# Kernel optimization log

Hardware: AMD Instinct MI355X
Metric: run time of the kernel (lower is better)

The kernel has to match this reference:

```python
import jax, jax.numpy as jnp
import numpy as np

B, S, T, H, E = 256, 512, 16, 1024, 512  # batch, src_len, trg_steps, hidden, emb_dim


def setup_inputs() -> dict:
    key = jax.random.key(0)
    ks = jax.random.split(key, 10)
    rn = lambda k, sh: jax.random.normal(k, sh, dtype=jnp.float32) * 0.05
    return {
        "trg_emb": rn(ks[0], (B, T, E)),
        "h0": rn(ks[1], (B, H)),
        "c0": rn(ks[2], (B, H)),
        "ctx": rn(ks[3], (B, S, H)),
        "src_len": jax.random.randint(ks[4], (B,), 1, S + 1, dtype=jnp.int32),
        "W_ih": rn(ks[5], (4 * H, E + H)),  # input-feeding: lstm in = emb + hidden
        "W_hh": rn(ks[6], (4 * H, H)),
        "b_ih": jnp.zeros((4 * H,), jnp.float32),
        "b_hh": jnp.zeros((4 * H,), jnp.float32),
        "W_in": rn(ks[7], (H, H)),    # attention linear_in (no bias)
        "W_out": rn(ks[8], (H, 2 * H)),  # attention linear_out (no bias)
    }


def reference(trg_emb, h0, c0, ctx, src_len, W_ih, W_hh, b_ih, b_hh, W_in, W_out):
    # mask[b, s] = s < src_len[b]
    mask = jnp.arange(S)[None, :] < src_len[:, None]  # (B, S)
    neg = jnp.float32(-1e9)

    def step(carry, emb_t):
        h, c, h_tilde = carry  # each (B, H); emb_t (B, E)
        # input feeding: concat target embedding with previous attentional vector
        x = jnp.concatenate([emb_t, h_tilde], axis=1)  # (B, E+H)
        gates = x @ W_ih.T + b_ih + h @ W_hh.T + b_hh  # (B, 4H), pytorch gate order i,f,g,o
        i, f, g, o = jnp.split(gates, 4, axis=1)
        i = jax.nn.sigmoid(i); f = jax.nn.sigmoid(f)
        g = jnp.tanh(g);       o = jax.nn.sigmoid(o)
        c = f * c + i * g
        h = o * jnp.tanh(c)
        # Luong soft-dot attention with src_len masking
        target = h @ W_in.T                                # (B, H)
        scores = jnp.einsum('bsh,bh->bs', ctx, target)     # (B, S)
        scores = jnp.where(mask, scores, neg)
        attn = jax.nn.softmax(scores, axis=-1)
        weighted = jnp.einsum('bs,bsh->bh', attn, ctx)     # (B, H)
        h_tilde = jnp.tanh(jnp.concatenate([weighted, h], axis=1) @ W_out.T)
        return (h, c, h_tilde), h_tilde

    # initial h_tilde = init_hidden[0] (per the original code)
    (h_f, c_f, _), hs = jax.lax.scan(step, (h0, c0, h0), jnp.swapaxes(trg_emb, 0, 1))
    output = jnp.swapaxes(hs, 0, 1)  # (B, T, H)
    return output, h_f, c_f
```

## Files before the change

### kernel.cpp

```cpp
#include <hip/hip_runtime.h>
#include <cstdint>
#include <cstddef>


#define B_ 256
#define S_ 512
#define T_ 16
#define H_ 1024
#define E_ 512
#define NBUF 4

typedef unsigned short u16;
using short8 = __attribute__((ext_vector_type(8))) short;
using f32x4  = __attribute__((ext_vector_type(4))) float;

__device__ __forceinline__ float bf2f(u16 u) {
  union { uint32_t i; float f; } v; v.i = ((uint32_t)u) << 16; return v.f;
}
__device__ __forceinline__ u16 f2bf(float f) {
  union { uint32_t i; float f; } v; v.f = f;
  uint32_t r = v.i + 0x7fffu + ((v.i >> 16) & 1u);
  return (u16)(r >> 16);
}
__device__ __forceinline__ float sigmoidf_(float x) { return 1.f / (1.f + __expf(-x)); }

__device__ __forceinline__ void gload_lds16(const void* g, void* l) {
  __builtin_amdgcn_global_load_lds(
      (const __attribute__((address_space(1))) void*)g,
      (__attribute__((address_space(3))) void*)l, 16, 0, 0);
}

struct Reg3 { const u16* A; int lda; const u16* B; int ldb; int kt; };

template <int EPI>
__global__ __launch_bounds__(128) void gemm_k(Reg3 r0, Reg3 r1, Reg3 r2,
                                              int nmb,
                                              float* __restrict__ Cf,
                                              u16* __restrict__ Cb,
                                              const float* __restrict__ bsum,
                                              float* __restrict__ cst,
                                              float* __restrict__ h32o,
                                              u16* __restrict__ hbfo,
                                              const int tstep) {
  __shared__ u16 smA[NBUF][64 * 64];
  __shared__ u16 smB[NBUF][64 * 64];
  const int tid = threadIdx.x;
  const int lane = tid & 63;
  const int wave = tid >> 6;
  const int m0 = (blockIdx.x % nmb) * 64;
  const int n0 = (blockIdx.x / nmb) * 64;
  const int row16 = lane & 15;
  const int kg = lane >> 4;
  const int nt = r0.kt + r1.kt + r2.kt;

  auto stage = [&](int ti, int buf) {
    const int k01 = r0.kt + r1.kt;
    const u16* Ap = (ti < r0.kt) ? r0.A : (ti < k01) ? r1.A : r2.A;
    const u16* Bp = (ti < r0.kt) ? r0.B : (ti < k01) ? r1.B : r2.B;
    const int lda = (ti < r0.kt) ? r0.lda : (ti < k01) ? r1.lda : r2.lda;
    const int ldb = (ti < r0.kt) ? r0.ldb : (ti < k01) ? r1.ldb : r2.ldb;
    const int base = (ti < r0.kt) ? 0 : (ti < k01) ? r0.kt : k01;
    const int kr = (ti - base) << 6;
#pragma unroll
    for (int j = 0; j < 4; ++j) {
      const int c = j * 128 + tid;
      const int row = c >> 3, q = c & 7;
      gload_lds16(Ap + (size_t)(m0 + row) * lda + kr + ((q ^ (row & 7)) << 3),
                  (char*)&smA[buf][0] + (size_t)(j * 128 + wave * 64) * 16);
    }
#pragma unroll
    for (int j = 0; j < 4; ++j) {
      const int c = j * 128 + tid;
      const int row = c >> 3, q = c & 7;
      gload_lds16(Bp + (size_t)(n0 + row) * ldb + kr + ((q ^ (row & 7)) << 3),
                  (char*)&smB[buf][0] + (size_t)(j * 128 + wave * 64) * 16);
    }
  };

  f32x4 acc[4][2] = {};
  stage(0, 0);
  if (nt > 1) stage(1, 1);
  for (int ti = 0; ti < nt; ++ti) {
    const int buf = ti & 3;
    if (ti + 2 < nt) {
      stage(ti + 2, (ti + 2) & 3);
      asm volatile("s_waitcnt vmcnt(16)" ::: "memory");
    } else if (ti + 1 < nt) {
      asm volatile("s_waitcnt vmcnt(8)" ::: "memory");
    } else {
      asm volatile("s_waitcnt vmcnt(0)" ::: "memory");
    }
    __builtin_amdgcn_s_barrier();
    __builtin_amdgcn_sched_barrier(0);
#pragma unroll
    for (int ks = 0; ks < 2; ++ks) {
      short8 af[4], bfr[2];
#pragma unroll
      for (int mi = 0; mi < 4; ++mi) {
        const int R = mi * 16 + row16;
        af[mi] = *(const short8*)((const char*)&smA[buf][0] +
                                  (size_t)(((R << 3) | ((ks * 4 + kg) ^ (R & 7))) << 4));
      }
#pragma unroll
      for (int ni = 0; ni < 2; ++ni) {
        const int R = wave * 32 + ni * 16 + row16;
        bfr[ni] = *(const short8*)((const char*)&smB[buf][0] +
                                   (size_t)(((R << 3) | ((ks * 4 + kg) ^ (R & 7))) << 4));
      }
      asm volatile("s_waitcnt lgkmcnt(0)" ::: "memory");
      __builtin_amdgcn_sched_barrier(0);
#pragma unroll
      for (int mi = 0; mi < 4; ++mi)
#pragma unroll
        for (int ni = 0; ni < 2; ++ni)
          acc[mi][ni] = __builtin_amdgcn_mfma_f32_16x16x32_bf16(af[mi], bfr[ni], acc[mi][ni], 0, 0, 0);
      __builtin_amdgcn_sched_barrier(0);
    }
  }
#pragma unroll
  for (int mi = 0; mi < 4; ++mi) {
#pragma unroll
    for (int ni = 0; ni < 2; ++ni) {
#pragma unroll
      for (int r = 0; r < 4; ++r) {
        const int row = m0 + mi * 16 + (kg << 2) + r;
        const int col = n0 + wave * 32 + ni * 16 + row16;
        float v = acc[mi][ni][r];
        if (EPI == 2) {
          float tv = tanhf(v);
          Cf[(size_t)row * (T_ * H_) + (size_t)tstep * H_ + col] = tv;
          Cb[row * H_ + col] = f2bf(tv);
        } else {
          v += bsum[col];
          float v1 = __shfl_xor(v, 1);
          float v2 = __shfl_xor(v, 2);
          float v3 = __shfl_xor(v, 3);
          if ((lane & 3) == 0) {
            const int u = col >> 2;
            float iv = sigmoidf_(v);
            float fv = sigmoidf_(v1);
            float gv = tanhf(v2);
            float ov = sigmoidf_(v3);
            float cn = fv * cst[row * H_ + u] + iv * gv;
            float hn = ov * tanhf(cn);
            cst[row * H_ + u] = cn;
            h32o[row * H_ + u] = hn;
            hbfo[row * H_ + u] = f2bf(hn);
          }
        }
      }
    }
  }
}

__device__ __forceinline__ int fidx(int lane, int j) {
  return (j << 6) + ((lane + (j << 2)) & 63);
}

__global__ __launch_bounds__(1024) void attn_k(const u16* __restrict__ hbf,
                                               const u16* __restrict__ WinT,
                                               const u16* __restrict__ ctxb,
                                               const int* __restrict__ src_len,
                                               u16* __restrict__ wwbf) {
  __shared__ float hsm[1024];
  __shared__ float tgtp[1024 + 64];
  __shared__ float facc[8][1024];
  __shared__ float fm[16], fl[16];
  const int b = blockIdx.x;
  const int tid = threadIdx.x;
  const int lane = tid & 63;
  const int wave = tid >> 6;
  const int len = src_len[b];

  hsm[tid] = bf2f(hbf[b * H_ + tid]);
  __syncthreads();

  {
    float a = 0.f;
    const u16* wp = WinT + tid * 8;
    for (int k8 = 0; k8 < 128; ++k8) {
      short8 wv = *(const short8*)(wp + (size_t)k8 * 8192);
      float4 h0v = *(const float4*)&hsm[k8 * 8];
      float4 h1v = *(const float4*)&hsm[k8 * 8 + 4];
      a += bf2f((u16)wv[0]) * h0v.x + bf2f((u16)wv[1]) * h0v.y
         + bf2f((u16)wv[2]) * h0v.z + bf2f((u16)wv[3]) * h0v.w
         + bf2f((u16)wv[4]) * h1v.x + bf2f((u16)wv[5]) * h1v.y
         + bf2f((u16)wv[6]) * h1v.z + bf2f((u16)wv[7]) * h1v.w;
    }
    tgtp[tid + (tid >> 4)] = a;
  }
  __syncthreads();

  float tg[16];
#pragma unroll
  for (int j = 0; j < 16; ++j) tg[j] = tgtp[lane * 17 + j];

  float m = -1e30f, l = 0.f;
  float acc[16];
#pragma unroll
  for (int j = 0; j < 16; ++j) acc[j] = 0.f;

  for (int s = wave; s < len; s += 16) {
    const u16* cr = ctxb + (((size_t)b * S_ + s) << 10) + (lane << 4);
    short8 v1 = *(const short8*)cr;
    short8 v2 = *(const short8*)(cr + 8);
    float cf[16];
#pragma unroll
    for (int j = 0; j < 8; ++j) { cf[j] = bf2f((u16)v1[j]); cf[8 + j] = bf2f((u16)v2[j]); }
    float x = 0.f;
#pragma unroll
    for (int j = 0; j < 16; ++j) x += cf[j] * tg[j];
#pragma unroll
    for (int off = 1; off < 64; off <<= 1) x += __shfl_xor(x, off);
    if (x > m) {
      float sc_ = __expf(m - x);
      l *= sc_;
#pragma unroll
      for (int j = 0; j < 16; ++j) acc[j] *= sc_;
      m = x;
    }
    float p = __expf(x - m);
    l += p;
#pragma unroll
    for (int j = 0; j < 16; ++j) acc[j] += p * cf[j];
  }

  if (wave >= 8) {
#pragma unroll
    for (int j = 0; j < 16; ++j) facc[wave - 8][fidx(lane, j)] = acc[j];
    if (lane == 0) { fm[wave] = m; fl[wave] = l; }
  }
  __syncthreads();
  if (wave < 8) {
    float pm = fm[8 + wave];
    float pl = fl[8 + wave];
    float M = fmaxf(m, pm);
    float e1 = __expf(m - M);
    float e2 = __expf(pm - M);
#pragma unroll
    for (int j = 0; j < 16; ++j) {
      float pv = facc[wave][fidx(lane, j)];
      facc[wave][fidx(lane, j)] = acc[j] * e1 + pv * e2;
    }
    if (lane == 0) { fm[wave] = M; fl[wave] = l * e1 + pl * e2; }
  }
  __syncthreads();
  float mstar = -1e30f;
#pragma unroll
  for (int w = 0; w < 8; ++w) mstar = fmaxf(mstar, fm[w]);
  float lsum = 0.f, asum = 0.f;
  const int ri = fidx(tid >> 4, tid & 15);
#pragma unroll
  for (int w = 0; w < 8; ++w) {
    float e = __expf(fm[w] - mstar);
    lsum += fl[w] * e;
    asum += facc[w][ri] * e;
  }
  wwbf[b * H_ + tid] = f2bf(asum / lsum);
}

__global__ __launch_bounds__(256) void convert_all(
    const float* __restrict__ W_ih, const float* __restrict__ W_hh,
    const float* __restrict__ W_in, const float* __restrict__ W_out,
    const float* __restrict__ trg_emb, const float* __restrict__ ctx,
    const float* __restrict__ b_ih, const float* __restrict__ b_hh,
    const float* __restrict__ h0, const float* __restrict__ c0,
    u16* __restrict__ wWih, u16* __restrict__ wWhh, u16* __restrict__ wWinT,
    u16* __restrict__ wWout, u16* __restrict__ wemb, u16* __restrict__ wctx,
    float* __restrict__ wbsum, u16* __restrict__ wh0, u16* __restrict__ whtbf,
    float* __restrict__ wc) {
  const int gtid = blockIdx.x * 256 + threadIdx.x;
  const int GSZ = 2048 * 256;
  auto cvt4 = [](float4 v) {
    ushort4 o; o.x = f2bf(v.x); o.y = f2bf(v.y); o.z = f2bf(v.z); o.w = f2bf(v.w);
    return o;
  };
  for (int i = gtid; i < 1572864; i += GSZ) {
    const int r = i / 384, c4 = i - r * 384;
    const int rp = ((r & 1023) << 2) + (r >> 10);
    ((ushort4*)wWih)[(size_t)rp * 384 + c4] = cvt4(((const float4*)W_ih)[i]);
  }
  for (int i = gtid; i < 1048576; i += GSZ) {
    const int r = i >> 8, c4 = i & 255;
    const int rp = ((r & 1023) << 2) + (r >> 10);
    ((ushort4*)wWhh)[(size_t)rp * 256 + c4] = cvt4(((const float4*)W_hh)[i]);
  }
  for (int i = gtid; i < 524288; i += GSZ)
    ((ushort4*)wWout)[i] = cvt4(((const float4*)W_out)[i]);
  for (int i = gtid; i < 524288; i += GSZ)
    ((ushort4*)wemb)[i] = cvt4(((const float4*)trg_emb)[i]);
  for (int i = gtid; i < 131072; i += GSZ) {
    const int n = i >> 7, k8 = i & 127;
    const float* s = W_in + (size_t)n * 1024 + k8 * 8;
    ushort4* d = (ushort4*)(wWinT + (size_t)k8 * 8192 + n * 8);
    d[0] = cvt4(*(const float4*)s);
    d[1] = cvt4(*(const float4*)(s + 4));
  }
  for (int i = gtid; i < 33554432; i += GSZ)
    ((ushort4*)wctx)[i] = cvt4(((const float4*)ctx)[i]);
  if (gtid < 4096) {
    const int cp = ((gtid & 1023) << 2) + (gtid >> 10);
    wbsum[cp] = b_ih[gtid] + b_hh[gtid];
  }
  for (int i = gtid; i < 262144; i += GSZ) {
    u16 hb = f2bf(h0[i]);
    wh0[i] = hb;
    whtbf[i] = hb;
    wc[i] = c0[i];
  }
}

extern "C" void kernel_launch(void* const* d_in, const int* in_sizes, int n_in,
                              void* d_out, int out_size, void* d_ws, size_t ws_size,
                              hipStream_t stream) {
  const float* trg_emb = (const float*)d_in[0];
  const float* h0      = (const float*)d_in[1];
  const float* c0      = (const float*)d_in[2];
  const float* ctx     = (const float*)d_in[3];
  const int*   src_len = (const int*)d_in[4];
  const float* W_ih    = (const float*)d_in[5];
  const float* W_hh    = (const float*)d_in[6];
  const float* b_ih    = (const float*)d_in[7];
  const float* b_hh    = (const float*)d_in[8];
  const float* W_in    = (const float*)d_in[9];
  const float* W_out   = (const float*)d_in[10];
  float* out = (float*)d_out;

  char* w = (char*)d_ws;
  size_t off = 0;
  auto alloc = [&](size_t bytes) { char* p = w + off; off += bytes; return p; };
  u16*   wWih  = (u16*)  alloc(12582912);
  u16*   wWhh  = (u16*)  alloc(8388608);
  u16*   wWinT = (u16*)  alloc(2097152);
  u16*   wWout = (u16*)  alloc(4194304);
  u16*   wemb  = (u16*)  alloc(4194304);
  float* wbsum = (float*)alloc(16384);
  float* wh32  = (float*)alloc(1048576);
  float* wc    = (float*)alloc(1048576);
  u16*   wh0   = (u16*)  alloc(524288);
  u16*   wh1   = (u16*)  alloc(524288);
  u16*   whtbf = (u16*)  alloc(524288);
  u16*   wwbf  = (u16*)  alloc(524288);
  u16*   wctx  = (u16*)  alloc(268435456);
  (void)ws_size;

  convert_all<<<dim3(2048), dim3(256), 0, stream>>>(
      W_ih, W_hh, W_in, W_out, trg_emb, ctx, b_ih, b_hh, h0, c0,
      wWih, wWhh, wWinT, wWout, wemb, wctx, wbsum, wh0, whtbf, wc);

  Reg3 rz = { nullptr, 0, nullptr, 0, 0 };
  for (int t = 0; t < T_; ++t) {
    const u16* hcur = (t & 1) ? wh1 : wh0;
    u16* hnxt = (t & 1) ? wh0 : wh1;
    Reg3 g0 = { wemb + (size_t)t * E_, T_ * E_, wWih,      E_ + H_, 8 };
    Reg3 g1 = { whtbf,                 H_,      wWih + E_, E_ + H_, 16 };
    Reg3 g2 = { hcur,                  H_,      wWhh,      H_,      16 };
    gemm_k<3><<<dim3(256), dim3(128), 0, stream>>>(
        g0, g1, g2, 4, nullptr, nullptr, wbsum, wc, wh32, hnxt, 0);
    attn_k<<<dim3(B_), dim3(1024), 0, stream>>>(hnxt, wWinT, wctx, src_len, wwbf);
    Reg3 o0 = { wwbf, H_, wWout,      2 * H_, 16 };
    Reg3 o1 = { hnxt, H_, wWout + H_, 2 * H_, 16 };
    gemm_k<2><<<dim3(64), dim3(128), 0, stream>>>(
        o0, o1, rz, 4, out, whtbf, nullptr, nullptr, nullptr, nullptr, t);
  }
  hipMemcpyAsync(out + (size_t)B_ * T_ * H_, wh32, (size_t)B_ * H_ * sizeof(float),
                 hipMemcpyDeviceToDevice, stream);
  hipMemcpyAsync(out + (size_t)B_ * T_ * H_ + B_ * H_, wc, (size_t)B_ * H_ * sizeof(float),
                 hipMemcpyDeviceToDevice, stream);
}
```

Before: 2.237 ms.

## Compact ctx to valid rows and move attention linear_in to MFMA GEMM

Converts only the first src_len rows of each batch's ctx to bf16 and packs them contiguously using a prefix-sum offset table, so the one-time conversion reads and writes less data and the attention loop streams a denser buffer. Replaces the per-block scalar W_in matvec inside attn_k with a separate MFMA GEMM launch producing the target vector in bf16. This adds two small kernels plus one extra launch per step, and rounds the target to bf16 before it is used for scoring.

Result: faster. 2.096 ms (-6.3%).

```diff
diff --git a/kernel.cpp b/kernel.cpp
--- a/kernel.cpp
+++ b/kernel.cpp
@@ -21,6 +21,10 @@
   union { uint32_t i; float f; } v; v.f = f;
   uint32_t r = v.i + 0x7fffu + ((v.i >> 16) & 1u);
   return (u16)(r >> 16);
+}
+__device__ __forceinline__ ushort4 cvt4bf(float4 v) {
+  ushort4 o; o.x = f2bf(v.x); o.y = f2bf(v.y); o.z = f2bf(v.z); o.w = f2bf(v.w);
+  return o;
 }
 __device__ __forceinline__ float sigmoidf_(float x) { return 1.f / (1.f + __expf(-x)); }
 
@@ -126,7 +130,9 @@
         const int row = m0 + mi * 16 + (kg << 2) + r;
         const int col = n0 + wave * 32 + ni * 16 + row16;
         float v = acc[mi][ni][r];
-        if (EPI == 2) {
+        if (EPI == 1) {
+          Cb[row * H_ + col] = f2bf(v);
+        } else if (EPI == 2) {
           float tv = tanhf(v);
           Cf[(size_t)row * (T_ * H_) + (size_t)tstep * H_ + col] = tv;
           Cb[row * H_ + col] = f2bf(tv);
@@ -157,13 +163,11 @@
   return (j << 6) + ((lane + (j << 2)) & 63);
 }
 
-__global__ __launch_bounds__(1024) void attn_k(const u16* __restrict__ hbf,
-                                               const u16* __restrict__ WinT,
-                                               const u16* __restrict__ ctxb,
+__global__ __launch_bounds__(1024) void attn_k(const u16* __restrict__ tgt,
+                                               const u16* __restrict__ ctxc,
+                                               const int* __restrict__ offs,
                                                const int* __restrict__ src_len,
                                                u16* __restrict__ wwbf) {
-  __shared__ float hsm[1024];
-  __shared__ float tgtp[1024 + 64];
   __shared__ float facc[8][1024];
   __shared__ float fm[16], fl[16];
   const int b = blockIdx.x;
@@ -171,29 +175,16 @@
   const int lane = tid & 63;
   const int wave = tid >> 6;
   const int len = src_len[b];
-
-  hsm[tid] = bf2f(hbf[b * H_ + tid]);
-  __syncthreads();
-
+  const u16* cb = ctxc + ((size_t)offs[b] << 10);
+
+  float tg[16];
   {
-    float a = 0.f;
-    const u16* wp = WinT + tid * 8;
-    for (int k8 = 0; k8 < 128; ++k8) {
-      short8 wv = *(const short8*)(wp + (size_t)k8 * 8192);
-      float4 h0v = *(const float4*)&hsm[k8 * 8];
-      float4 h1v = *(const float4*)&hsm[k8 * 8 + 4];
-      a += bf2f((u16)wv[0]) * h0v.x + bf2f((u16)wv[1]) * h0v.y
-         + bf2f((u16)wv[2]) * h0v.z + bf2f((u16)wv[3]) * h0v.w
-         + bf2f((u16)wv[4]) * h1v.x + bf2f((u16)wv[5]) * h1v.y
-         + bf2f((u16)wv[6]) * h1v.z + bf2f((u16)wv[7]) * h1v.w;
-    }
-    tgtp[tid + (tid >> 4)] = a;
-  }
-  __syncthreads();
-
-  float tg[16];
-#pragma unroll
-  for (int j = 0; j < 16; ++j) tg[j] = tgtp[lane * 17 + j];
+    const u16* tp = tgt + b * H_ + lane * 16;
+    short8 v1 = *(const short8*)tp;
+    short8 v2 = *(const short8*)(tp + 8);
+#pragma unroll
+    for (int j = 0; j < 8; ++j) { tg[j] = bf2f((u16)v1[j]); tg[8 + j] = bf2f((u16)v2[j]); }
+  }
 
   float m = -1e30f, l = 0.f;
   float acc[16];
@@ -201,7 +192,7 @@
   for (int j = 0; j < 16; ++j) acc[j] = 0.f;
 
   for (int s = wave; s < len; s += 16) {
-    const u16* cr = ctxb + (((size_t)b * S_ + s) << 10) + (lane << 4);
+    const u16* cr = cb + ((size_t)s << 10) + (lane << 4);
     short8 v1 = *(const short8*)cr;
     short8 v2 = *(const short8*)(cr + 8);
     float cf[16];
@@ -259,45 +250,61 @@
   wwbf[b * H_ + tid] = f2bf(asum / lsum);
 }
 
+__global__ __launch_bounds__(256) void scan_k(const int* __restrict__ len,
+                                              int* __restrict__ offs) {
+  __shared__ int tmp[256];
+  const int tid = threadIdx.x;
+  const int v = len[tid];
+  tmp[tid] = v;
+  __syncthreads();
+  for (int off = 1; off < 256; off <<= 1) {
+    int t = (tid >= off) ? tmp[tid - off] : 0;
+    __syncthreads();
+    tmp[tid] += t;
+    __syncthreads();
+  }
+  offs[tid] = tmp[tid] - v;
+}
+
+__global__ __launch_bounds__(256) void ctx_compact(const float* __restrict__ ctx,
+                                                   const int* __restrict__ src_len,
+                                                   const int* __restrict__ offs,
+                                                   u16* __restrict__ ctxc) {
+  const int b = blockIdx.x;
+  const int n4 = src_len[b] << 8;
+  const float4* s = (const float4*)(ctx + ((size_t)b << 19));
+  ushort4* d = (ushort4*)(ctxc + ((size_t)offs[b] << 10));
+  for (int i = threadIdx.x; i < n4; i += 256) d[i] = cvt4bf(s[i]);
+}
+
 __global__ __launch_bounds__(256) void convert_all(
     const float* __restrict__ W_ih, const float* __restrict__ W_hh,
     const float* __restrict__ W_in, const float* __restrict__ W_out,
-    const float* __restrict__ trg_emb, const float* __restrict__ ctx,
+    const float* __restrict__ trg_emb,
     const float* __restrict__ b_ih, const float* __restrict__ b_hh,
     const float* __restrict__ h0, const float* __restrict__ c0,
-    u16* __restrict__ wWih, u16* __restrict__ wWhh, u16* __restrict__ wWinT,
-    u16* __restrict__ wWout, u16* __restrict__ wemb, u16* __restrict__ wctx,
+    u16* __restrict__ wWih, u16* __restrict__ wWhh, u16* __restrict__ wWin,
+    u16* __restrict__ wWout, u16* __restrict__ wemb,
     float* __restrict__ wbsum, u16* __restrict__ wh0, u16* __restrict__ whtbf,
     float* __restrict__ wc) {
   const int gtid = blockIdx.x * 256 + threadIdx.x;
-  const int GSZ = 2048 * 256;
-  auto cvt4 = [](float4 v) {
-    ushort4 o; o.x = f2bf(v.x); o.y = f2bf(v.y); o.z = f2bf(v.z); o.w = f2bf(v.w);
-    return o;
-  };
+  const int GSZ = 1024 * 256;
   for (int i = gtid; i < 1572864; i += GSZ) {
     const int r = i / 384, c4 = i - r * 384;
     const int rp = ((r & 1023) << 2) + (r >> 10);
-    ((ushort4*)wWih)[(size_t)rp * 384 + c4] = cvt4(((const float4*)W_ih)[i]);
+    ((ushort4*)wWih)[(size_t)rp * 384 + c4] = cvt4bf(((const float4*)W_ih)[i]);
   }
   for (int i = gtid; i < 1048576; i += GSZ) {
     const int r = i >> 8, c4 = i & 255;
     const int rp = ((r & 1023) << 2) + (r >> 10);
-    ((ushort4*)wWhh)[(size_t)rp * 256 + c4] = cvt4(((const float4*)W_hh)[i]);
-  }
+    ((ushort4*)wWhh)[(size_t)rp * 256 + c4] = cvt4bf(((const float4*)W_hh)[i]);
+  }
+  for (int i = gtid; i < 262144; i += GSZ)
+    ((ushort4*)wWin)[i] = cvt4bf(((const float4*)W_in)[i]);
   for (int i = gtid; i < 524288; i += GSZ)
-    ((ushort4*)wWout)[i] = cvt4(((const float4*)W_out)[i]);
+    ((ushort4*)wWout)[i] = cvt4bf(((const float4*)W_out)[i]);
   for (int i = gtid; i < 524288; i += GSZ)
-    ((ushort4*)wemb)[i] = cvt4(((const float4*)trg_emb)[i]);
-  for (int i = gtid; i < 131072; i += GSZ) {
-    const int n = i >> 7, k8 = i & 127;
-    const float* s = W_in + (size_t)n * 1024 + k8 * 8;
-    ushort4* d = (ushort4*)(wWinT + (size_t)k8 * 8192 + n * 8);
-    d[0] = cvt4(*(const float4*)s);
-    d[1] = cvt4(*(const float4*)(s + 4));
-  }
-  for (int i = gtid; i < 33554432; i += GSZ)
-    ((ushort4*)wctx)[i] = cvt4(((const float4*)ctx)[i]);
+    ((ushort4*)wemb)[i] = cvt4bf(((const float4*)trg_emb)[i]);
   if (gtid < 4096) {
     const int cp = ((gtid & 1023) << 2) + (gtid >> 10);
     wbsum[cp] = b_ih[gtid] + b_hh[gtid];
@@ -331,7 +338,7 @@
   auto alloc = [&](size_t bytes) { char* p = w + off; off += bytes; return p; };
   u16*   wWih  = (u16*)  alloc(12582912);
   u16*   wWhh  = (u16*)  alloc(8388608);
-  u16*   wWinT = (u16*)  alloc(2097152);
+  u16*   wWin  = (u16*)  alloc(2097152);
   u16*   wWout = (u16*)  alloc(4194304);
   u16*   wemb  = (u16*)  alloc(4194304);
   float* wbsum = (float*)alloc(16384);
@@ -340,13 +347,17 @@
   u16*   wh0   = (u16*)  alloc(524288);
   u16*   wh1   = (u16*)  alloc(524288);
   u16*   whtbf = (u16*)  alloc(524288);
+  u16*   wtgt  = (u16*)  alloc(524288);
   u16*   wwbf  = (u16*)  alloc(524288);
-  u16*   wctx  = (u16*)  alloc(268435456);
+  int*   woffs = (int*)  alloc(1024);
+  u16*   wctxc = (u16*)  alloc(268435456);
   (void)ws_size;
 
-  convert_all<<<dim3(2048), dim3(256), 0, stream>>>(
-      W_ih, W_hh, W_in, W_out, trg_emb, ctx, b_ih, b_hh, h0, c0,
-      wWih, wWhh, wWinT, wWout, wemb, wctx, wbsum, wh0, whtbf, wc);
+  scan_k<<<dim3(1), dim3(256), 0, stream>>>(src_len, woffs);
+  convert_all<<<dim3(1024), dim3(256), 0, stream>>>(
+      W_ih, W_hh, W_in, W_out, trg_emb, b_ih, b_hh, h0, c0,
+      wWih, wWhh, wWin, wWout, wemb, wbsum, wh0, whtbf, wc);
+  ctx_compact<<<dim3(B_), dim3(256), 0, stream>>>(ctx, src_len, woffs, wctxc);
 
   Reg3 rz = { nullptr, 0, nullptr, 0, 0 };
   for (int t = 0; t < T_; ++t) {
@@ -357,7 +368,10 @@
     Reg3 g2 = { hcur,                  H_,      wWhh,      H_,      16 };
     gemm_k<3><<<dim3(256), dim3(128), 0, stream>>>(
         g0, g1, g2, 4, nullptr, nullptr, wbsum, wc, wh32, hnxt, 0);
-    attn_k<<<dim3(B_), dim3(1024), 0, stream>>>(hnxt, wWinT, wctx, src_len, wwbf);
+    Reg3 i0 = { hnxt, H_, wWin, H_, 16 };
+    gemm_k<1><<<dim3(64), dim3(128), 0, stream>>>(
+        i0, rz, rz, 4, nullptr, wtgt, nullptr, nullptr, nullptr, nullptr, 0);
+    attn_k<<<dim3(B_), dim3(1024), 0, stream>>>(wtgt, wctxc, woffs, src_len, wwbf);
     Reg3 o0 = { wwbf, H_, wWout,      2 * H_, 16 };
     Reg3 o1 = { hnxt, H_, wWout + H_, 2 * H_, 16 };
     gemm_k<2><<<dim3(64), dim3(128), 0, stream>>>(
```
